# Kernel optimization log

Hardware: AMD Instinct MI355X
Metric: run time of the kernel (lower is better)

Reference implementation:

```python
import jax, jax.numpy as jnp
import numpy as np

N, E, B = 20000, 320000, 64
IN_DIM, HID, HEADS, NGF = 128, 64, 4, 9
NEG_SLOPE = 0.2
SET2SET_STEPS = 3


def _gat_conv(x, src, dst, W, a_src, a_dst, b, n):
    # PyG GATConv (eval mode): h = xW split into heads, edge score =
    # LeakyReLU(a_src.h[src] + a_dst.h[dst]), softmax over edges per dst node,
    # weighted scatter-sum of h[src], heads concatenated, + bias.
    H, C = a_src.shape
    h = (x @ W).reshape(n, H, C)                       # [N,H,C]
    s = jnp.sum(h * a_src, axis=-1)                    # [N,H]
    d = jnp.sum(h * a_dst, axis=-1)                    # [N,H]
    e = jax.nn.leaky_relu(s[src] + d[dst], NEG_SLOPE)  # [E,H]
    emax = jax.ops.segment_max(e, dst, num_segments=n)
    ex = jnp.exp(e - emax[dst])
    denom = jax.ops.segment_sum(ex, dst, num_segments=n)
    alpha = ex / (denom[dst] + 1e-16)                  # [E,H]
    out = jax.ops.segment_sum(h[src] * alpha[..., None], dst, num_segments=n)
    return out.reshape(n, H * C) + b


def _set2set(x, batch, Wih, Whh, bih, bhh, n_graphs):
    # Set2Set pooling: LSTM(q_star) -> attention over nodes per graph -> readout.
    d = x.shape[1]
    h = jnp.zeros((n_graphs, d), x.dtype)
    c = jnp.zeros((n_graphs, d), x.dtype)
    q_star = jnp.zeros((n_graphs, 2 * d), x.dtype)
    for _ in range(SET2SET_STEPS):
        gates = q_star @ Wih.T + bih + h @ Whh.T + bhh   # [B,4d], torch gate order i,f,g,o
        i, f, g, o = jnp.split(gates, 4, axis=1)
        c = jax.nn.sigmoid(f) * c + jax.nn.sigmoid(i) * jnp.tanh(g)
        h = jax.nn.sigmoid(o) * jnp.tanh(c)
        q = h                                            # [B,d]
        e = jnp.sum(x * q[batch], axis=-1)               # [N]
        emax = jax.ops.segment_max(e, batch, num_segments=n_graphs)
        a = jnp.exp(e - emax[batch])
        a = a / (jax.ops.segment_sum(a, batch, num_segments=n_graphs)[batch] + 1e-16)
        r = jax.ops.segment_sum(a[:, None] * x, batch, num_segments=n_graphs)  # [B,d]
        q_star = jnp.concatenate([q, r], axis=1)
    return q_star


def setup_inputs() -> dict:
    key = jax.random.key(0)
    ks = jax.random.split(key, 20)
    sc = 0.1
    inp = {
        "x": jax.random.normal(ks[0], (N, IN_DIM), jnp.float32),
        "edge_index": jax.random.randint(ks[1], (2, E), 0, N, dtype=jnp.int32),
        "batch": jnp.sort(jax.random.randint(ks[2], (N,), 0, B, dtype=jnp.int32)),
        "graph_features": jax.random.normal(ks[3], (B, NGF), jnp.float32),
        "W1": sc * jax.random.normal(ks[4], (IN_DIM, HEADS * HID), jnp.float32),
        "a_src1": sc * jax.random.normal(ks[5], (HEADS, HID), jnp.float32),
        "a_dst1": sc * jax.random.normal(ks[6], (HEADS, HID), jnp.float32),
        "b1": jnp.zeros((HEADS * HID,), jnp.float32),
        "W2": sc * jax.random.normal(ks[7], (HEADS * HID, HEADS * HID), jnp.float32),
        "a_src2": sc * jax.random.normal(ks[8], (HEADS, HID), jnp.float32),
        "a_dst2": sc * jax.random.normal(ks[9], (HEADS, HID), jnp.float32),
        "b2": jnp.zeros((HEADS * HID,), jnp.float32),
        "W3": sc * jax.random.normal(ks[10], (HEADS * HID, 2 * HID), jnp.float32),
        "a_src3": sc * jax.random.normal(ks[11], (1, 2 * HID), jnp.float32),
        "a_dst3": sc * jax.random.normal(ks[12], (1, 2 * HID), jnp.float32),
        "b3": jnp.zeros((2 * HID,), jnp.float32),
        "Wih": sc * jax.random.normal(ks[13], (4 * 2 * HID, 4 * HID), jnp.float32),
        "Whh": sc * jax.random.normal(ks[14], (4 * 2 * HID, 2 * HID), jnp.float32),
        "bih": jnp.zeros((4 * 2 * HID,), jnp.float32),
        "bhh": jnp.zeros((4 * 2 * HID,), jnp.float32),
        "gW1": sc * jax.random.normal(ks[15], (NGF, HID), jnp.float32),
        "gb1": jnp.zeros((HID,), jnp.float32),
        "gW2": sc * jax.random.normal(ks[16], (HID, HID // 2), jnp.float32),
        "gb2": jnp.zeros((HID // 2,), jnp.float32),
        "mW1": sc * jax.random.normal(ks[17], (2 * (2 * HID) + HID // 2, 128), jnp.float32),
        "mb1": jnp.zeros((128,), jnp.float32),
        "mW2": sc * jax.random.normal(ks[18], (128, 4), jnp.float32),
        "mb2": jnp.zeros((4,), jnp.float32),
    }
    return inp


def reference(x, edge_index, batch, graph_features,
              W1, a_src1, a_dst1, b1,
              W2, a_src2, a_dst2, b2,
              W3, a_src3, a_dst3, b3,
              Wih, Whh, bih, bhh,
              gW1, gb1, gW2, gb2,
              mW1, mb1, mW2, mb2):
    n = x.shape[0]
    # PyG GATConv default add_self_loops=True
    loops = jnp.arange(n, dtype=edge_index.dtype)
    src = jnp.concatenate([edge_index[0], loops])
    dst = jnp.concatenate([edge_index[1], loops])
    h = jax.nn.elu(_gat_conv(x, src, dst, W1, a_src1, a_dst1, b1, n))
    h = jax.nn.elu(_gat_conv(h, src, dst, W2, a_src2, a_dst2, b2, n))
    h = jax.nn.elu(_gat_conv(h, src, dst, W3, a_src3, a_dst3, b3, n))
    pooled = _set2set(h, batch, Wih, Whh, bih, bhh, B)              # [B, 256]
    gf = jax.nn.relu(graph_features @ gW1 + gb1) @ gW2 + gb2        # [B, 32]
    z = jnp.concatenate([pooled, gf], axis=1)                       # [B, 288]
    scores = jax.nn.relu(z @ mW1 + mb1) @ mW2 + mb2                 # [B, 4]
    return scores
```

## Files before the change

### kernel.cpp

```cpp
#include <hip/hip_runtime.h>
#include <hip/hip_bf16.h>
#include <math.h>

#define NEG_SLOPE 0.2f

__device__ __forceinline__ float sigmoidf(float x){ return 1.f/(1.f+expf(-x)); }

__global__ void init_kernel(int* counts, int* gstart, int* gend,
                            float* rsum, float* lsum, int n, int b){
  int i = blockIdx.x*blockDim.x + threadIdx.x;
  if (i < n) counts[i] = 0;
  if (i < b){ gstart[i] = 0; gend[i] = 0; }
  if (i < 3*b*128) rsum[i] = 0.f;
  if (i < 3*b) lsum[i] = 0.f;
}

__global__ void build_kernel(const int* __restrict__ ei, const int* __restrict__ batch,
                             int* counts, int* gstart, int* gend, int E, int n){
  int i = blockIdx.x*blockDim.x + threadIdx.x;
  if (i < E) atomicAdd(&counts[ei[E+i]], 1);
  if (i < n){
    int b = batch[i];
    if (i == 0 || batch[i-1] != b) gstart[b] = i;
    if (i == n-1 || batch[i+1] != b) gend[b] = i+1;
  }
}

__global__ void scan_kernel(const int* __restrict__ counts, int* offs, int* cursor, int n){
  const int T = 1024;
  int tid = threadIdx.x;
  int chunk = (n + T - 1)/T;
  int base = tid*chunk;
  int local = 0;
  for (int i=0;i<chunk;i++){ int idx=base+i; if (idx<n) local += counts[idx]; }
  __shared__ int ss[T];
  ss[tid]=local; __syncthreads();
  for (int off=1; off<T; off<<=1){
    int v = (tid>=off)? ss[tid-off] : 0;
    __syncthreads();
    ss[tid]+=v;
    __syncthreads();
  }
  int run = ss[tid]-local;
  for (int i=0;i<chunk;i++){
    int idx=base+i;
    if (idx<n){ offs[idx]=run; cursor[idx]=run; run += counts[idx]; }
  }
  if (tid==T-1) offs[n]=run;
}

__global__ void fill_kernel(const int* __restrict__ ei, int* cursor, int* csr, int E){
  int i = blockIdx.x*blockDim.x + threadIdx.x;
  if (i<E){
    int dst = ei[E+i];
    int pos = atomicAdd(&cursor[dst],1);
    csr[pos] = ei[i];
  }
}

__global__ __launch_bounds__(256) void gemm64x128(const float* __restrict__ A,
                                                  const float* __restrict__ B,
                                                  float* __restrict__ C,
                                                  int M, int K, int N){
  __shared__ float As[16][64];
  __shared__ float Bs[16][128];
  int tid = threadIdx.x;
  int bm = blockIdx.x*64, bn = blockIdx.y*128;
  int ar = tid>>2, ak=(tid&3)*4;
  int br = tid>>4, bc=(tid&15)*8;
  int ty = tid>>4, tx = tid&15;
  float acc[4][8] = {};
  for (int k0=0; k0<K; k0+=16){
    float4 av = make_float4(0,0,0,0);
    if (bm+ar < M) av = *reinterpret_cast<const float4*>(A + (size_t)(bm+ar)*K + k0 + ak);
    const float* bp = B + (size_t)(k0+br)*N + bn + bc;
    float4 b0 = *reinterpret_cast<const float4*>(bp);
    float4 b1 = *reinterpret_cast<const float4*>(bp+4);
    As[ak+0][ar]=av.x; As[ak+1][ar]=av.y; As[ak+2][ar]=av.z; As[ak+3][ar]=av.w;
    *reinterpret_cast<float4*>(&Bs[br][bc])   = b0;
    *reinterpret_cast<float4*>(&Bs[br][bc+4]) = b1;
    __syncthreads();
    #pragma unroll
    for (int kk=0; kk<16; kk++){
      float4 av0 = *reinterpret_cast<float4*>(&As[kk][ty*4]);
      float4 bv0 = *reinterpret_cast<float4*>(&Bs[kk][tx*4]);
      float4 bv1 = *reinterpret_cast<float4*>(&Bs[kk][64+tx*4]);
      float a[4] = {av0.x,av0.y,av0.z,av0.w};
      float b[8] = {bv0.x,bv0.y,bv0.z,bv0.w, bv1.x,bv1.y,bv1.z,bv1.w};
      #pragma unroll
      for (int i=0;i<4;i++)
        #pragma unroll
        for (int j=0;j<8;j++)
          acc[i][j] += a[i]*b[j];
    }
    __syncthreads();
  }
  #pragma unroll
  for (int i=0;i<4;i++){
    int row = bm + ty*4 + i;
    if (row < M){
      float* cp = C + (size_t)row*N + bn;
      *reinterpret_cast<float4*>(cp + tx*4)    = make_float4(acc[i][0],acc[i][1],acc[i][2],acc[i][3]);
      *reinterpret_cast<float4*>(cp + 64+tx*4) = make_float4(acc[i][4],acc[i][5],acc[i][6],acc[i][7]);
    }
  }
}

template<int H, int C>
__global__ void sd_kernel(const float* __restrict__ h, const float* __restrict__ asrc,
                          const float* __restrict__ adst, float* __restrict__ s,
                          float* __restrict__ d, int n_nodes){
  int wave = threadIdx.x >> 6, lane = threadIdx.x & 63;
  int n = blockIdx.x*4 + wave;
  if (n >= n_nodes) return;
  const float* hn = h + (size_t)n*H*C;
  #pragma unroll
  for (int hd=0; hd<H; ++hd){
    float ps=0.f, pd=0.f;
    for (int c=lane; c<C; c+=64){
      float v = hn[hd*C+c];
      ps += v*asrc[hd*C+c];
      pd += v*adst[hd*C+c];
    }
    #pragma unroll
    for (int off=32; off; off>>=1){ ps += __shfl_down(ps,off); pd += __shfl_down(pd,off); }
    if (lane==0){ s[n*H+hd]=ps; d[n*H+hd]=pd; }
  }
}

template<int H, int C>
__global__ __launch_bounds__(256) void agg_kernel(
    const float* __restrict__ hbuf, const float* __restrict__ s,
    const float* __restrict__ d, const int* __restrict__ offs,
    const int* __restrict__ csr, const float* __restrict__ bias,
    float* __restrict__ y, int n_nodes){
  constexpr int HC = H*C;
  constexpr int VEC = HC/64;
  int n = blockIdx.x;
  int tid = threadIdx.x;
  int wave = tid>>6, lane = tid&63;
  __shared__ float sdst[H];
  __shared__ float sl[H];
  __shared__ float sw[64*H];
  __shared__ int ssrc[64];
  __shared__ float facc[4][HC];
  if (tid < H) sdst[tid] = d[n*H+tid];
  int start = offs[n];
  int cnt = offs[n+1]-start;
  int cnt1 = cnt+1;
  __syncthreads();
  float acc[VEC] = {};
  float lp[H];
  #pragma unroll
  for (int h=0;h<H;h++) lp[h]=0.f;
  for (int base=0; base<cnt1; base+=64){
    int nchunk = min(64, cnt1-base);
    if (tid < nchunk){
      int i = base+tid;
      int src = (i==cnt) ? n : csr[start+i];
      ssrc[tid]=src;
      if (H == 4){
        float4 sv = *reinterpret_cast<const float4*>(s + (size_t)src*4);
        float ev[4] = {sv.x, sv.y, sv.z, sv.w};
        #pragma unroll
        for (int h=0;h<4;h++){
          float e = ev[h] + sdst[h];
          e = e>=0.f ? e : NEG_SLOPE*e;
          float w = expf(e);
          sw[tid*4+h]=w;
          lp[h]+=w;
        }
      } else {
        float e = s[src] + sdst[0];
        e = e>=0.f ? e : NEG_SLOPE*e;
        float w = expf(e);
        sw[tid]=w;
        lp[0]+=w;
      }
    }
    __syncthreads();
    for (int j=wave; j<nchunk; j+=4){
      int src = ssrc[j];
      const float* hp = hbuf + (size_t)src*HC + lane*VEC;
      if (VEC == 4){
        float wt = sw[j*H + (lane>>4)];
        float4 hv = *reinterpret_cast<const float4*>(hp);
        acc[0]+=wt*hv.x; acc[1]+=wt*hv.y; acc[2]+=wt*hv.z; acc[3]+=wt*hv.w;
      } else {
        float wt = sw[j];
        float2 hv = *reinterpret_cast<const float2*>(hp);
        acc[0]+=wt*hv.x; acc[1]+=wt*hv.y;
      }
    }
    __syncthreads();
  }
  if (wave==0){
    #pragma unroll
    for (int off=32; off; off>>=1)
      #pragma unroll
      for (int h=0;h<H;h++) lp[h] += __shfl_down(lp[h],off);
    if (lane==0)
      #pragma unroll
      for (int h=0;h<H;h++) sl[h]=lp[h];
  }
  #pragma unroll
  for (int v=0;v<VEC;v++) facc[wave][lane*VEC+v] = acc[v];
  __syncthreads();
  if (tid < HC){
    float a = facc[0][tid]+facc[1][tid]+facc[2][tid]+facc[3][tid];
    int head = tid / C;
    float o = a/(sl[head]+1e-16f) + bias[tid];
    y[(size_t)n*HC+tid] = o>0.f ? o : expm1f(o);
  }
}

__global__ __launch_bounds__(256) void read_kernel(
    const float* __restrict__ x, const float* __restrict__ q,
    const int* __restrict__ batch,
    float* __restrict__ rsum, float* __restrict__ lsum, int N){
  int tid = threadIdx.x;
  int wave = tid>>6, lane = tid&63;
  int c0 = blockIdx.x*32;
  if (c0 >= N) return;
  __shared__ float ws[32];
  __shared__ int gb[32];
  if (tid < 32 && c0+tid < N) gb[tid] = batch[c0+tid];
  __syncthreads();
  #pragma unroll
  for (int j=0;j<8;j++){
    int k = wave*8 + j;
    int i = c0 + k;
    if (i < N){
      int g = gb[k];
      float2 xv = *reinterpret_cast<const float2*>(x + (size_t)i*128 + lane*2);
      float2 qv = *reinterpret_cast<const float2*>(q + (size_t)g*128 + lane*2);
      float p = xv.x*qv.x + xv.y*qv.y;
      #pragma unroll
      for (int off=32; off; off>>=1) p += __shfl_down(p, off);
      if (lane==0) ws[k] = expf(p);
    }
  }
  __syncthreads();
  if (tid < 128){
    int col = tid;
    int endi = min(c0+32, N);
    int curg = gb[0];
    float acc = 0.f, lacc = 0.f;
    for (int i=c0; i<endi; ++i){
      int g = gb[i-c0];
      if (g != curg){
        atomicAdd(&rsum[curg*128+col], acc);
        if (col==0) atomicAdd(&lsum[curg], lacc);
        acc = 0.f; lacc = 0.f; curg = g;
      }
      float w = ws[i-c0];
      acc += w * x[(size_t)i*128+col];
      lacc += w;
    }
    atomicAdd(&rsum[curg*128+col], acc);
    if (col==0) atomicAdd(&lsum[curg], lacc);
  }
}

template<int STEP>
__global__ __launch_bounds__(256) void s2s_step_kernel(
    const float* __restrict__ rsum, const float* __restrict__ lsum,
    float* __restrict__ hc, float* __restrict__ qbuf,
    const float* __restrict__ Wih, const float* __restrict__ Whh,
    const float* __restrict__ bih, const float* __restrict__ bhh,
    const float* __restrict__ gfeat,
    const float* __restrict__ gW1, const float* __restrict__ gb1,
    const float* __restrict__ gW2, const float* __restrict__ gb2,
    const float* __restrict__ mW1, const float* __restrict__ mb1,
    const float* __restrict__ mW2, const float* __restrict__ mb2,
    float* __restrict__ out, int B){
  int b = blockIdx.x, tid = threadIdx.x;
  __shared__ float qs[256];

  if (STEP > 0){
    if (tid < 128){
      const float* rs = rsum + (size_t)(STEP-1)*B*128 + (size_t)b*128;
      float ls = lsum[(STEP-1)*B + b];
      qs[tid]     = qbuf[b*128+tid];
      qs[128+tid] = rs[tid] / (ls + 1e-16f);
    }
    __syncthreads();
  }

  if (STEP < 3){
    __shared__ float hs[128], gsh[512];
    if (STEP > 0){ if (tid<128) hs[tid] = hc[(size_t)b*128+tid]; }
    __syncthreads();
    #pragma unroll
    for (int p=0;p<2;p++){
      int j = tid + p*256;
      float a = bih[j] + bhh[j];
      if (STEP > 0){
        const float* wi = Wih + (size_t)j*256;
        for (int k=0;k<256;k+=4)
          a += qs[k]*wi[k] + qs[k+1]*wi[k+1] + qs[k+2]*wi[k+2] + qs[k+3]*wi[k+3];
        const float* wh = Whh + (size_t)j*128;
        for (int k=0;k<128;k+=4)
          a += hs[k]*wh[k] + hs[k+1]*wh[k+1] + hs[k+2]*wh[k+2] + hs[k+3]*wh[k+3];
      }
      gsh[j] = a;
    }
    __syncthreads();
    if (tid < 128){
      float cprev = (STEP==0) ? 0.f : hc[(size_t)(B+b)*128+tid];
      float ig = sigmoidf(gsh[tid]);
      float fg = sigmoidf(gsh[128+tid]);
      float gg = tanhf(gsh[256+tid]);
      float og = sigmoidf(gsh[384+tid]);
      float c2 = fg*cprev + ig*gg;
      float h2 = og*tanhf(c2);
      hc[(size_t)b*128+tid] = h2;
      hc[(size_t)(B+b)*128+tid] = c2;
      qbuf[b*128+tid] = h2;
    }
  } else {
    __shared__ float z[288], gf1[64], hid[128];
    z[tid] = qs[tid];
    if (tid < 64){
      float a = gb1[tid];
      for (int k=0;k<9;k++) a += gfeat[b*9+k]*gW1[k*64+tid];
      gf1[tid] = a>0.f ? a : 0.f;
    }
    __syncthreads();
    if (tid < 32){
      float a = gb2[tid];
      for (int k=0;k<64;k++) a += gf1[k]*gW2[k*32+tid];
      z[256+tid] = a;
    }
    __syncthreads();
    if (tid < 128){
      float a = mb1[tid];
      for (int k=0;k<288;k++) a += z[k]*mW1[(size_t)k*128+tid];
      hid[tid] = a>0.f ? a : 0.f;
    }
    __syncthreads();
    if (tid < 4){
      float a = mb2[tid];
      for (int k=0;k<128;k++) a += hid[k]*mW2[k*4+tid];
      out[b*4+tid] = a;
    }
  }
}

extern "C" void kernel_launch(void* const* d_in, const int* in_sizes, int n_in,
                              void* d_out, int out_size, void* d_ws, size_t ws_size,
                              hipStream_t stream) {
  const float* x     = (const float*)d_in[0];
  const int*   ei    = (const int*)d_in[1];
  const int*   batch = (const int*)d_in[2];
  const float* gfeat = (const float*)d_in[3];
  const float* W1    = (const float*)d_in[4];
  const float* as1   = (const float*)d_in[5];
  const float* ad1   = (const float*)d_in[6];
  const float* b1    = (const float*)d_in[7];
  const float* W2    = (const float*)d_in[8];
  const float* as2   = (const float*)d_in[9];
  const float* ad2   = (const float*)d_in[10];
  const float* b2    = (const float*)d_in[11];
  const float* W3    = (const float*)d_in[12];
  const float* as3   = (const float*)d_in[13];
  const float* ad3   = (const float*)d_in[14];
  const float* b3    = (const float*)d_in[15];
  const float* Wih   = (const float*)d_in[16];
  const float* Whh   = (const float*)d_in[17];
  const float* bih   = (const float*)d_in[18];
  const float* bhh   = (const float*)d_in[19];
  const float* gW1   = (const float*)d_in[20];
  const float* gb1   = (const float*)d_in[21];
  const float* gW2   = (const float*)d_in[22];
  const float* gb2   = (const float*)d_in[23];
  const float* mW1   = (const float*)d_in[24];
  const float* mb1   = (const float*)d_in[25];
  const float* mW2   = (const float*)d_in[26];
  const float* mb2   = (const float*)d_in[27];

  const int N = in_sizes[0]/128;
  const int E = in_sizes[1]/2;
  const int B = in_sizes[3]/9;

  char* ws = (char*)d_ws;
  size_t off = 0;
  auto alloc = [&](size_t bytes)->char*{
    char* p = ws + off;
    off += (bytes + 255) & ~(size_t)255;
    return p;
  };
  float* hbuf   = (float*)alloc((size_t)N*256*4);
  float* ybuf1  = (float*)alloc((size_t)N*256*4);
  float* ybuf2  = (float*)alloc((size_t)N*256*4);
  float* sbuf   = (float*)alloc((size_t)N*4*4);
  float* dbuf   = (float*)alloc((size_t)N*4*4);
  int*   counts = (int*)alloc((size_t)N*4);
  int*   offs   = (int*)alloc((size_t)(N+1)*4);
  int*   cursor = (int*)alloc((size_t)N*4);
  int*   csr    = (int*)alloc((size_t)E*4);
  int*   gstart = (int*)alloc((size_t)B*4);
  int*   gend   = (int*)alloc((size_t)B*4);
  float* hcbuf  = (float*)alloc((size_t)2*B*128*4);
  float* qbuf   = (float*)alloc((size_t)B*128*4);
  float* rsum   = (float*)alloc((size_t)3*B*128*4);
  float* lsum   = (float*)alloc((size_t)3*B*4);

  int nInit = max(N, 3*B*128);
  init_kernel<<<(nInit+255)/256, 256, 0, stream>>>(counts, gstart, gend,
                                                   rsum, lsum, N, B);
  int gridEN = (max(E,N)+255)/256;
  build_kernel<<<gridEN, 256, 0, stream>>>(ei, batch, counts, gstart, gend, E, N);
  scan_kernel<<<1, 1024, 0, stream>>>(counts, offs, cursor, N);
  fill_kernel<<<(E+255)/256, 256, 0, stream>>>(ei, cursor, csr, E);

  int gm = (N+63)/64;
  gemm64x128<<<dim3(gm,2), 256, 0, stream>>>(x, W1, hbuf, N, 128, 256);
  sd_kernel<4,64><<<(N+3)/4, 256, 0, stream>>>(hbuf, as1, ad1, sbuf, dbuf, N);
  agg_kernel<4,64><<<N, 256, 0, stream>>>(hbuf, sbuf, dbuf, offs, csr, b1, ybuf1, N);
  gemm64x128<<<dim3(gm,2), 256, 0, stream>>>(ybuf1, W2, hbuf, N, 256, 256);
  sd_kernel<4,64><<<(N+3)/4, 256, 0, stream>>>(hbuf, as2, ad2, sbuf, dbuf, N);
  agg_kernel<4,64><<<N, 256, 0, stream>>>(hbuf, sbuf, dbuf, offs, csr, b2, ybuf2, N);
  gemm64x128<<<dim3(gm,1), 256, 0, stream>>>(ybuf2, W3, hbuf, N, 256, 128);
  sd_kernel<1,128><<<(N+3)/4, 256, 0, stream>>>(hbuf, as3, ad3, sbuf, dbuf, N);
  agg_kernel<1,128><<<N, 256, 0, stream>>>(hbuf, sbuf, dbuf, offs, csr, b3, ybuf1, N);

  int gr = (N+31)/32;
  s2s_step_kernel<0><<<B, 256, 0, stream>>>(rsum, lsum, hcbuf, qbuf,
      Wih, Whh, bih, bhh, gfeat, gW1, gb1, gW2, gb2, mW1, mb1, mW2, mb2, (float*)d_out, B);
  read_kernel<<<gr, 256, 0, stream>>>(ybuf1, qbuf, batch, rsum + 0*(size_t)B*128, lsum + 0*B, N);
  s2s_step_kernel<1><<<B, 256, 0, stream>>>(rsum, lsum, hcbuf, qbuf,
      Wih, Whh, bih, bhh, gfeat, gW1, gb1, gW2, gb2, mW1, mb1, mW2, mb2, (float*)d_out, B);
  read_kernel<<<gr, 256, 0, stream>>>(ybuf1, qbuf, batch, rsum + 1*(size_t)B*128, lsum + 1*B, N);
  s2s_step_kernel<2><<<B, 256, 0, stream>>>(rsum, lsum, hcbuf, qbuf,
      Wih, Whh, bih, bhh, gfeat, gW1, gb1, gW2, gb2, mW1, mb1, mW2, mb2, (float*)d_out, B);
  read_kernel<<<gr, 256, 0, stream>>>(ybuf1, qbuf, batch, rsum + 2*(size_t)B*128, lsum + 2*B, N);
  s2s_step_kernel<3><<<B, 256, 0, stream>>>(rsum, lsum, hcbuf, qbuf,
      Wih, Whh, bih, bhh, gfeat, gW1, gb1, gW2, gb2, mW1, mb1, mW2, mb2, (float*)d_out, B);
}
```

Before: 551.5 us.

## Replace fp32 SIMT GEMMs with split-bf16 MFMA GEMMs and split-packed activations

Swaps the three fp32 FMA-based GEMMs for a 128x128-tile kernel built on bf16 16x16x32 MFMA instructions. Each fp32 value is stored as an interleaved bf16 hi/lo pair, which doubles K. The input x and the weights are converted by new kernels, and the first two aggregation kernels write their outputs directly in split form. The intent is to move GEMM work onto the matrix cores. In exchange it adds conversion passes and padded buffers. The interleaved pairing only forms hi*hi + lo*lo products and drops the cross terms, so accuracy is only somewhat better than plain bf16 and numerical tolerance is at risk.

```diff
diff --git a/kernel.cpp b/kernel.cpp
--- a/kernel.cpp
+++ b/kernel.cpp
@@ -4,15 +4,30 @@
 
 #define NEG_SLOPE 0.2f
 
+typedef __attribute__((ext_vector_type(8))) short bf16x8;
+typedef __attribute__((ext_vector_type(4))) float f32x4;
+
 __device__ __forceinline__ float sigmoidf(float x){ return 1.f/(1.f+expf(-x)); }
 
+__device__ __forceinline__ unsigned pack_split(float v){
+  __hip_bfloat16 hi = __float2bfloat16(v);
+  float rem = v - __bfloat162float(hi);
+  __hip_bfloat16 lo = __float2bfloat16(rem);
+  unsigned short uh = __builtin_bit_cast(unsigned short, hi);
+  unsigned short ul = __builtin_bit_cast(unsigned short, lo);
+  return (unsigned)uh | ((unsigned)ul << 16);
+}
+
 __global__ void init_kernel(int* counts, int* gstart, int* gend,
-                            float* rsum, float* lsum, int n, int b){
+                            float* rsum, float* lsum,
+                            int* pad1, int* pad2, int npadints,
+                            int n, int b){
   int i = blockIdx.x*blockDim.x + threadIdx.x;
   if (i < n) counts[i] = 0;
   if (i < b){ gstart[i] = 0; gend[i] = 0; }
   if (i < 3*b*128) rsum[i] = 0.f;
   if (i < 3*b) lsum[i] = 0.f;
+  if (i < npadints){ pad1[i] = 0; pad2[i] = 0; }
 }
 
 __global__ void build_kernel(const int* __restrict__ ei, const int* __restrict__ batch,
@@ -58,50 +73,84 @@
   }
 }
 
-__global__ __launch_bounds__(256) void gemm64x128(const float* __restrict__ A,
-                                                  const float* __restrict__ B,
-                                                  float* __restrict__ C,
-                                                  int M, int K, int N){
-  __shared__ float As[16][64];
-  __shared__ float Bs[16][128];
+__global__ void convert_x(const float* __restrict__ x, unsigned* __restrict__ xs,
+                          int Nrows, int Mpad){
+  int idx = blockIdx.x*blockDim.x + threadIdx.x;
+  if (idx >= Mpad*128) return;
+  int r = idx >> 7;
+  float v = (r < Nrows) ? x[idx] : 0.f;
+  xs[idx] = pack_split(v);
+}
+
+__global__ void convert_wT(const float* __restrict__ W, unsigned* __restrict__ WT,
+                           int K, int N){
+  int idx = blockIdx.x*blockDim.x + threadIdx.x;
+  if (idx >= K*N) return;
+  int k = idx / N, n = idx - k*N;
+  WT[(size_t)n*K + k] = pack_split(W[idx]);
+}
+
+__global__ __launch_bounds__(256) void gemm_bf16(
+    const short* __restrict__ A, const short* __restrict__ BT,
+    float* __restrict__ C, int M, int Ktot, int N){
+  __shared__ short As[128][72];
+  __shared__ short Bs[128][72];
   int tid = threadIdx.x;
-  int bm = blockIdx.x*64, bn = blockIdx.y*128;
-  int ar = tid>>2, ak=(tid&3)*4;
-  int br = tid>>4, bc=(tid&15)*8;
-  int ty = tid>>4, tx = tid&15;
-  float acc[4][8] = {};
-  for (int k0=0; k0<K; k0+=16){
-    float4 av = make_float4(0,0,0,0);
-    if (bm+ar < M) av = *reinterpret_cast<const float4*>(A + (size_t)(bm+ar)*K + k0 + ak);
-    const float* bp = B + (size_t)(k0+br)*N + bn + bc;
-    float4 b0 = *reinterpret_cast<const float4*>(bp);
-    float4 b1 = *reinterpret_cast<const float4*>(bp+4);
-    As[ak+0][ar]=av.x; As[ak+1][ar]=av.y; As[ak+2][ar]=av.z; As[ak+3][ar]=av.w;
-    *reinterpret_cast<float4*>(&Bs[br][bc])   = b0;
-    *reinterpret_cast<float4*>(&Bs[br][bc+4]) = b1;
-    __syncthreads();
-    #pragma unroll
-    for (int kk=0; kk<16; kk++){
-      float4 av0 = *reinterpret_cast<float4*>(&As[kk][ty*4]);
-      float4 bv0 = *reinterpret_cast<float4*>(&Bs[kk][tx*4]);
-      float4 bv1 = *reinterpret_cast<float4*>(&Bs[kk][64+tx*4]);
-      float a[4] = {av0.x,av0.y,av0.z,av0.w};
-      float b[8] = {bv0.x,bv0.y,bv0.z,bv0.w, bv1.x,bv1.y,bv1.z,bv1.w};
+  int wave = tid>>6, lane = tid&63;
+  int quad = lane>>4, l16 = lane&15;
+  int wm = wave>>1, wn = wave&1;
+  int bm = blockIdx.x*128, bn = blockIdx.y*128;
+  f32x4 acc[4][4];
+  #pragma unroll
+  for (int i=0;i<4;i++)
+    #pragma unroll
+    for (int j=0;j<4;j++)
+      acc[i][j] = (f32x4){0.f,0.f,0.f,0.f};
+  int rs = tid>>3;
+  int seg = (tid&7)*8;
+  for (int k0=0; k0<Ktot; k0+=64){
+    int4 ra[4], rb[4];
+    #pragma unroll
+    for (int p=0;p<4;p++){
+      int r = p*32 + rs;
+      ra[p] = *(const int4*)(A + (size_t)(bm+r)*Ktot + k0 + seg);
+      rb[p] = *(const int4*)(BT + (size_t)(bn+r)*Ktot + k0 + seg);
+    }
+    __syncthreads();
+    #pragma unroll
+    for (int p=0;p<4;p++){
+      int r = p*32 + rs;
+      *(int4*)&As[r][seg] = ra[p];
+      *(int4*)&Bs[r][seg] = rb[p];
+    }
+    __syncthreads();
+    #pragma unroll
+    for (int kk=0;kk<2;kk++){
+      bf16x8 af[4], bf[4];
       #pragma unroll
-      for (int i=0;i<4;i++)
+      for (int f=0;f<4;f++){
+        af[f] = *(bf16x8*)&As[wm*64 + f*16 + l16][kk*32 + quad*8];
+        bf[f] = *(bf16x8*)&Bs[wn*64 + f*16 + l16][kk*32 + quad*8];
+      }
+      #pragma unroll
+      for (int mf=0;mf<4;mf++)
         #pragma unroll
-        for (int j=0;j<8;j++)
-          acc[i][j] += a[i]*b[j];
-    }
-    __syncthreads();
-  }
+        for (int nf=0;nf<4;nf++)
+          acc[mf][nf] = __builtin_amdgcn_mfma_f32_16x16x32_bf16(af[mf], bf[nf], acc[mf][nf], 0,0,0);
+    }
+  }
+  int col0 = bn + wn*64 + l16;
   #pragma unroll
-  for (int i=0;i<4;i++){
-    int row = bm + ty*4 + i;
-    if (row < M){
-      float* cp = C + (size_t)row*N + bn;
-      *reinterpret_cast<float4*>(cp + tx*4)    = make_float4(acc[i][0],acc[i][1],acc[i][2],acc[i][3]);
-      *reinterpret_cast<float4*>(cp + 64+tx*4) = make_float4(acc[i][4],acc[i][5],acc[i][6],acc[i][7]);
+  for (int mf=0;mf<4;mf++){
+    int row0 = bm + wm*64 + mf*16 + quad*4;
+    #pragma unroll
+    for (int r=0;r<4;r++){
+      int row = row0 + r;
+      if (row < M){
+        #pragma unroll
+        for (int nf=0;nf<4;nf++)
+          C[(size_t)row*N + col0 + nf*16] = acc[mf][nf][r];
+      }
     }
   }
 }
@@ -128,12 +177,12 @@
   }
 }
 
-template<int H, int C>
+template<int H, int C, bool SPLIT>
 __global__ __launch_bounds__(256) void agg_kernel(
     const float* __restrict__ hbuf, const float* __restrict__ s,
     const float* __restrict__ d, const int* __restrict__ offs,
     const int* __restrict__ csr, const float* __restrict__ bias,
-    float* __restrict__ y, int n_nodes){
+    float* __restrict__ yf, unsigned* __restrict__ ys, int n_nodes){
   constexpr int HC = H*C;
   constexpr int VEC = HC/64;
   int n = blockIdx.x;
@@ -210,7 +259,12 @@
     float a = facc[0][tid]+facc[1][tid]+facc[2][tid]+facc[3][tid];
     int head = tid / C;
     float o = a/(sl[head]+1e-16f) + bias[tid];
-    y[(size_t)n*HC+tid] = o>0.f ? o : expm1f(o);
+    o = o>0.f ? o : expm1f(o);
+    if (SPLIT){
+      ys[(size_t)n*HC + tid] = pack_split(o);
+    } else {
+      yf[(size_t)n*HC + tid] = o;
+    }
   }
 }
 
@@ -382,6 +436,7 @@
   const int N = in_sizes[0]/128;
   const int E = in_sizes[1]/2;
   const int B = in_sizes[3]/9;
+  const int Mpad = ((N + 127)/128)*128;
 
   char* ws = (char*)d_ws;
   size_t off = 0;
@@ -390,9 +445,14 @@
     off += (bytes + 255) & ~(size_t)255;
     return p;
   };
-  float* hbuf   = (float*)alloc((size_t)N*256*4);
-  float* ybuf1  = (float*)alloc((size_t)N*256*4);
-  float* ybuf2  = (float*)alloc((size_t)N*256*4);
+  float*    hbuf    = (float*)alloc((size_t)N*256*4);
+  unsigned* xsplit  = (unsigned*)alloc((size_t)Mpad*128*4);
+  unsigned* ysplit1 = (unsigned*)alloc((size_t)Mpad*256*4);
+  unsigned* ysplit2 = (unsigned*)alloc((size_t)Mpad*256*4);
+  float*    ybuf    = (float*)alloc((size_t)N*128*4);
+  unsigned* WT1     = (unsigned*)alloc((size_t)128*256*4);
+  unsigned* WT2     = (unsigned*)alloc((size_t)256*256*4);
+  unsigned* WT3     = (unsigned*)alloc((size_t)256*128*4);
   float* sbuf   = (float*)alloc((size_t)N*4*4);
   float* dbuf   = (float*)alloc((size_t)N*4*4);
   int*   counts = (int*)alloc((size_t)N*4);
@@ -406,35 +466,42 @@
   float* rsum   = (float*)alloc((size_t)3*B*128*4);
   float* lsum   = (float*)alloc((size_t)3*B*4);
 
-  int nInit = max(N, 3*B*128);
+  int npadints = (Mpad - N)*256;
+  int nInit = max(max(N, 3*B*128), npadints);
   init_kernel<<<(nInit+255)/256, 256, 0, stream>>>(counts, gstart, gend,
-                                                   rsum, lsum, N, B);
+      rsum, lsum, (int*)(ysplit1 + (size_t)N*256), (int*)(ysplit2 + (size_t)N*256),
+      npadints, N, B);
   int gridEN = (max(E,N)+255)/256;
   build_kernel<<<gridEN, 256, 0, stream>>>(ei, batch, counts, gstart, gend, E, N);
   scan_kernel<<<1, 1024, 0, stream>>>(counts, offs, cursor, N);
   fill_kernel<<<(E+255)/256, 256, 0, stream>>>(ei, cursor, csr, E);
 
-  int gm = (N+63)/64;
-  gemm64x128<<<dim3(gm,2), 256, 0, stream>>>(x, W1, hbuf, N, 128, 256);
+  convert_x<<<(Mpad*128+255)/256, 256, 0, stream>>>(x, xsplit, N, Mpad);
+  convert_wT<<<(128*256+255)/256, 256, 0, stream>>>(W1, WT1, 128, 256);
+  convert_wT<<<(256*256+255)/256, 256, 0, stream>>>(W2, WT2, 256, 256);
+  convert_wT<<<(256*128+255)/256, 256, 0, stream>>>(W3, WT3, 256, 128);
+
+  int gm = Mpad/128;
+  gemm_bf16<<<dim3(gm,2), 256, 0, stream>>>((const short*)xsplit, (const short*)WT1, hbuf, N, 256, 256);
   sd_kernel<4,64><<<(N+3)/4, 256, 0, stream>>>(hbuf, as1, ad1, sbuf, dbuf, N);
-  agg_kernel<4,64><<<N, 256, 0, stream>>>(hbuf, sbuf, dbuf, offs, csr, b1, ybuf1, N);
-  gemm64x128<<<dim3(gm,2), 256, 0, stream>>>(ybuf1, W2, hbuf, N, 256, 256);
+  agg_kernel<4,64,true><<<N, 256, 0, stream>>>(hbuf, sbuf, dbuf, offs, csr, b1, nullptr, ysplit1, N);
+  gemm_bf16<<<dim3(gm,2), 256, 0, stream>>>((const short*)ysplit1, (const short*)WT2, hbuf, N, 512, 256);
   sd_kernel<4,64><<<(N+3)/4, 256, 0, stream>>>(hbuf, as2, ad2, sbuf, dbuf, N);
-  agg_kernel<4,64><<<N, 256, 0, stream>>>(hbuf, sbuf, dbuf, offs, csr, b2, ybuf2, N);
-  gemm64x128<<<dim3(gm,1), 256, 0, stream>>>(ybuf2, W3, hbuf, N, 256, 128);
+  agg_kernel<4,64,true><<<N, 256, 0, stream>>>(hbuf, sbuf, dbuf, offs, csr, b2, nullptr, ysplit2, N);
+  gemm_bf16<<<dim3(gm,1), 256, 0, stream>>>((const short*)ysplit2, (const short*)WT3, hbuf, N, 512, 128);
   sd_kernel<1,128><<<(N+3)/4, 256, 0, stream>>>(hbuf, as3, ad3, sbuf, dbuf, N);
-  agg_kernel<1,128><<<N, 256, 0, stream>>>(hbuf, sbuf, dbuf, offs, csr, b3, ybuf1, N);
+  agg_kernel<1,128,false><<<N, 256, 0, stream>>>(hbuf, sbuf, dbuf, offs, csr, b3, ybuf, nullptr, N);
 
   int gr = (N+31)/32;
   s2s_step_kernel<0><<<B, 256, 0, stream>>>(rsum, lsum, hcbuf, qbuf,
       Wih, Whh, bih, bhh, gfeat, gW1, gb1, gW2, gb2, mW1, mb1, mW2, mb2, (float*)d_out, B);
-  read_kernel<<<gr, 256, 0, stream>>>(ybuf1, qbuf, batch, rsum + 0*(size_t)B*128, lsum + 0*B, N);
+  read_kernel<<<gr, 256, 0, stream>>>(ybuf, qbuf, batch, rsum + 0*(size_t)B*128, lsum + 0*B, N);
   s2s_step_kernel<1><<<B, 256, 0, stream>>>(rsum, lsum, hcbuf, qbuf,
       Wih, Whh, bih, bhh, gfeat, gW1, gb1, gW2, gb2, mW1, mb1, mW2, mb2, (float*)d_out, B);
-  read_kernel<<<gr, 256, 0, stream>>>(ybuf1, qbuf, batch, rsum + 1*(size_t)B*128, lsum + 1*B, N);
+  read_kernel<<<gr, 256, 0, stream>>>(ybuf, qbuf, batch, rsum + 1*(size_t)B*128, lsum + 1*B, N);
   s2s_step_kernel<2><<<B, 256, 0, stream>>>(rsum, lsum, hcbuf, qbuf,
       Wih, Whh, bih, bhh, gfeat, gW1, gb1, gW2, gb2, mW1, mb1, mW2, mb2, (float*)d_out, B);
-  read_kernel<<<gr, 256, 0, stream>>>(ybuf1, qbuf, batch, rsum + 2*(size_t)B*128, lsum + 2*B, N);
+  read_kernel<<<gr, 256, 0, stream>>>(ybuf, qbuf, batch, rsum + 2*(size_t)B*128, lsum + 2*B, N);
   s2s_step_kernel<3><<<B, 256, 0, stream>>>(rsum, lsum, hcbuf, qbuf,
       Wih, Whh, bih, bhh, gfeat, gW1, gb1, gW2, gb2, mW1, mb1, mW2, mb2, (float*)d_out, B);
 }
```

Result: slower. 572.0 us (+3.7%).
